# Kernel tuning notes

Measured on AMD Instinct MI355X. Metric: run time of the kernel, lower is better.

## Reference

```python
import jax, jax.numpy as jnp
import numpy as np

N_ORB = 1024    # Monte-Carlo orbits
NTIMES = 1024   # observation epochs
N_FZ = 24       # zodi flux grid points (uniform in log10)
N_KEZ = 6       # exozodi multipliers (sorted, searchsorted lookup)
N_TINT = 64     # integration times
N_ALPHA = 512   # separations (uniform in log10)


def setup_inputs() -> dict:
    key = jax.random.key(0)
    k1, k2, k3, k4 = jax.random.split(key, 4)
    fZs = jnp.logspace(-10.0, -7.0, N_FZ).astype(jnp.float32)
    alphas = jnp.logspace(-2.0, 1.0, N_ALPHA).astype(jnp.float32)
    kEZs = jnp.array([0.5, 1.0, 2.0, 5.0, 10.0, 20.0], dtype=jnp.float32)
    # grid already in the module's internal (n_fZ, n_kEZ, n_tint, n_alpha) layout
    grid = 25.0 + jax.random.normal(k1, (N_FZ, N_KEZ, N_TINT, N_ALPHA), dtype=jnp.float32)
    # alpha slightly exceeds [alphas[0], alphas[-1]] so geom_mask is exercised
    alpha = (10.0 ** jax.random.uniform(k2, (N_ORB, NTIMES), minval=-2.2, maxval=1.1)).astype(jnp.float32)
    dMag = (25.0 + jax.random.normal(k3, (N_ORB, NTIMES))).astype(jnp.float32)
    fZ_vals = (10.0 ** jax.random.uniform(k4, (NTIMES,), minval=-10.0, maxval=-7.0)).astype(jnp.float32)
    kEZ_val = jnp.float32(1.5)
    return dict(alpha=alpha, dMag=dMag, fZ_vals=fZ_vals, kEZ_val=kEZ_val,
                grid=grid, fZs=fZs, kEZs=kEZs, alphas=alphas)


def reference(alpha, dMag, fZ_vals, kEZ_val, grid, fZs, kEZs, alphas):
    """Faithful vectorized translation of dMag0Grid._pdet_alpha_dMag.

    alpha, dMag: (n_orb, ntimes); fZ_vals: (ntimes,); kEZ_val: scalar;
    grid: (n_fZ, n_kEZ, n_tint, n_alpha). Returns pdet (ntimes, n_tint).
    """
    n_fZ = fZs.shape[0]
    n_alpha = alphas.shape[0]
    log_fZs = jnp.log10(fZs)
    inv_log_fZ_step = 1.0 / (log_fZs[1] - log_fZs[0])
    log_alphas = jnp.log10(alphas)
    inv_log_alpha_step = 1.0 / (log_alphas[1] - log_alphas[0])

    geom_mask = (alpha >= alphas[0]) & (alpha <= alphas[-1])          # (n_orb, ntimes)

    fZ_ind = (jnp.log10(fZ_vals) - log_fZs[0]) * inv_log_fZ_step
    fZ0 = jnp.clip(jnp.floor(fZ_ind).astype(jnp.int32) + 1, 0, n_fZ - 2)  # (ntimes,)

    a_ind = (jnp.log10(alpha) - log_alphas[0]) * inv_log_alpha_step
    a0 = jnp.clip(a_ind.astype(jnp.int32), 0, n_alpha - 1)               # (n_orb, ntimes)
    dalpha = (a_ind - a0).astype(grid.dtype)

    kEZ_ind = jnp.searchsorted(kEZs, kEZ_val, side='right') - 1

    # lax.dynamic_slice clamps the start so the width-2 window fits:
    s = jnp.minimum(a0, n_alpha - 2)                                     # (n_orb, ntimes)

    g = jnp.take(grid, kEZ_ind, axis=1)                                  # (n_fZ, n_tint, n_alpha)
    g_f = g[fZ0]                                                          # (ntimes, n_tint, n_alpha)
    sT = s.T                                                              # (ntimes, n_orb)
    g0 = jnp.take_along_axis(g_f, sT[:, None, :], axis=2)                 # (ntimes, n_tint, n_orb)
    g1 = jnp.take_along_axis(g_f, (sT + 1)[:, None, :], axis=2)
    res = g0 + dalpha.T[:, None, :] * (g1 - g0)                           # (ntimes, n_tint, n_orb)

    dim = jnp.transpose(res, (2, 0, 1))                                   # (n_orb, ntimes, n_tint)
    det_mask = geom_mask[..., None] & jnp.signbit(dMag[..., None] - dim)
    pdet = det_mask.astype(jnp.float32).mean(axis=0)                      # (ntimes, n_tint)
    return pdet
```

## Files before the change

kernel.cpp:

```cpp
#include <hip/hip_runtime.h>
#include <math.h>

#define N_ORB   1024
#define NTIMES  1024
#define N_FZ    24
#define N_KEZ   6
#define N_TINT  64
#define N_ALPHA 512

#define GT_BYTES (N_FZ * N_ALPHA * N_TINT * 4)

__global__ __launch_bounds__(256) void stage_inputs(
    const float* __restrict__ grid, const float* __restrict__ kEZs,
    const float* __restrict__ kEZ_val_p, const float* __restrict__ alpha,
    const float* __restrict__ dMag, const float* __restrict__ alphas,
    float* __restrict__ gT, float4* __restrict__ P)
{
    __shared__ float lds[64 * 65];

    int b = blockIdx.x;
    if (b < 192) {
        float kv = kEZ_val_p[0];
        int cnt = 0;
#pragma unroll
        for (int i = 0; i < N_KEZ; ++i) cnt += (kEZs[i] <= kv) ? 1 : 0;
        int kez = cnt - 1;
        kez = kez < 0 ? 0 : (kez > N_KEZ - 1 ? N_KEZ - 1 : kez);

        int fz = b >> 3, sc = b & 7;
        int w = threadIdx.x >> 6, lane = threadIdx.x & 63;
        const float* gsrc = grid + ((size_t)fz * N_KEZ + kez) * N_TINT * N_ALPHA;

#pragma unroll
        for (int r = 0; r < 16; ++r) {
            int tint = w * 16 + r;
            lds[tint * 65 + lane] = gsrc[(size_t)tint * N_ALPHA + sc * 64 + lane];
        }
        __syncthreads();
#pragma unroll
        for (int r = 0; r < 16; ++r) {
            int sl = w * 16 + r;
            gT[((size_t)fz * N_ALPHA + sc * 64 + sl) * N_TINT + lane] = lds[lane * 65 + sl];
        }
    } else {
        float* da = lds;
        float* dm = lds + 1056;
        int*   of = (int*)(lds + 2112);

        int u = b - 192;
        int t0 = (u & 31) * 32, o0 = (u >> 5) * 32;
        int row = threadIdx.x >> 5, col = threadIdx.x & 31;

        float al0 = alphas[0], al1 = alphas[N_ALPHA - 1];
        float la0 = log10f(al0);
        float inv_step = 1.0f / (log10f(alphas[1]) - la0);

#pragma unroll
        for (int r = 0; r < 4; ++r) {
            int ol = r * 8 + row;
            size_t idx = (size_t)(o0 + ol) * NTIMES + t0 + col;
            float a = alpha[idx];
            float d = dMag[idx];
            float a_ind = (log10f(a) - la0) * inv_step;
            int a0i = (int)a_ind;
            a0i = a0i < 0 ? 0 : (a0i > N_ALPHA - 1 ? N_ALPHA - 1 : a0i);
            float dal = a_ind - (float)a0i;
            int s = a0i > N_ALPHA - 2 ? N_ALPHA - 2 : a0i;
            bool geom = (a >= al0) && (a <= al1);
            da[ol * 33 + col] = dal;
            dm[ol * 33 + col] = geom ? d : __builtin_inff();
            of[ol * 33 + col] = s * N_TINT;
        }
        __syncthreads();
#pragma unroll
        for (int r = 0; r < 4; ++r) {
            int tl = r * 8 + row;
            float4 v;
            v.x = da[col * 33 + tl];
            v.y = dm[col * 33 + tl];
            v.z = __int_as_float(of[col * 33 + tl]);
            v.w = 0.0f;
            P[(size_t)(t0 + tl) * N_ORB + o0 + col] = v;
        }
    }
}

__global__ __launch_bounds__(256) void pdet_main(
    const float* __restrict__ fZ_vals, const float* __restrict__ fZs,
    const float* __restrict__ gT, const float4* __restrict__ P,
    float* __restrict__ out)
{
    __shared__ float4 Psort[N_ORB];
    __shared__ int    hist[512];
    __shared__ int    histPS[512];
    __shared__ int    red[4 * 64];

    int t = blockIdx.x;
    int tid = threadIdx.x;
    int w = tid >> 6, lane = tid & 63;

    float lf0 = log10f(fZs[0]);
    float inv_f = 1.0f / (log10f(fZs[1]) - lf0);
    float fi = (log10f(fZ_vals[t]) - lf0) * inv_f;
    int f0 = (int)floorf(fi) + 1;
    f0 = f0 < 0 ? 0 : (f0 > N_FZ - 2 ? N_FZ - 2 : f0);

    const float*  gB = gT + (size_t)f0 * N_ALPHA * N_TINT;
    const float4* Pt = P + (size_t)t * N_ORB;

    hist[tid] = 0; hist[tid + 256] = 0;
    __syncthreads();

    float4 v[4];
    int    bin[4];
#pragma unroll
    for (int k = 0; k < 4; ++k) {
        v[k] = Pt[tid + k * 256];
        int s = __float_as_int(v[k].z) >> 6;
        bin[k] = isinf(v[k].y) ? 511 : s;
        atomicAdd(&hist[bin[k]], 1);
    }
    __syncthreads();

    if (tid < 64) {
        int pre[8]; int run = 0;
#pragma unroll
        for (int j = 0; j < 8; ++j) { pre[j] = run; run += hist[tid * 8 + j]; }
        int inc = run;
#pragma unroll
        for (int d = 1; d < 64; d <<= 1) {
            int n = __shfl_up(inc, d);
            if (lane >= d) inc += n;
        }
        int excl = inc - run;
#pragma unroll
        for (int j = 0; j < 8; ++j) histPS[tid * 8 + j] = excl + pre[j];
    }
    __syncthreads();

#pragma unroll
    for (int k = 0; k < 4; ++k) {
        int pos = atomicAdd(&histPS[bin[k]], 1);
        Psort[pos] = v[k];
    }
    __syncthreads();

    int q  = lane >> 4;
    int tg = (lane & 15) << 2;
    int base = w * 256;

    int c0 = 0, c1 = 0, c2 = 0, c3 = 0;

#pragma unroll 4
    for (int it = 0; it < 64; ++it) {
        float4 pd = Psort[base + it * 4 + q];
        float dal = pd.x, dm = pd.y;
        int offw = __float_as_int(pd.z);
        const float4* rowp = reinterpret_cast<const float4*>(gB + offw + tg);
        float4 g0 = rowp[0];
        float4 g1 = rowp[16];
        c0 += dm < fmaf(dal, g1.x - g0.x, g0.x);
        c1 += dm < fmaf(dal, g1.y - g0.y, g0.y);
        c2 += dm < fmaf(dal, g1.z - g0.z, g0.z);
        c3 += dm < fmaf(dal, g1.w - g0.w, g0.w);
    }

    c0 += __shfl_xor(c0, 16); c0 += __shfl_xor(c0, 32);
    c1 += __shfl_xor(c1, 16); c1 += __shfl_xor(c1, 32);
    c2 += __shfl_xor(c2, 16); c2 += __shfl_xor(c2, 32);
    c3 += __shfl_xor(c3, 16); c3 += __shfl_xor(c3, 32);

    if (lane < 16) {
        red[w * 64 + lane * 4 + 0] = c0;
        red[w * 64 + lane * 4 + 1] = c1;
        red[w * 64 + lane * 4 + 2] = c2;
        red[w * 64 + lane * 4 + 3] = c3;
    }
    __syncthreads();
    if (tid < 64) {
        int tot = red[tid] + red[64 + tid] + red[128 + tid] + red[192 + tid];
        out[(size_t)t * N_TINT + tid] = (float)tot * (1.0f / 1024.0f);
    }
}

extern "C" void kernel_launch(void* const* d_in, const int* in_sizes, int n_in,
                              void* d_out, int out_size, void* d_ws, size_t ws_size,
                              hipStream_t stream) {
    const float* alpha   = (const float*)d_in[0];
    const float* dMag    = (const float*)d_in[1];
    const float* fZ_vals = (const float*)d_in[2];
    const float* kEZ_val = (const float*)d_in[3];
    const float* grid    = (const float*)d_in[4];
    const float* fZs     = (const float*)d_in[5];
    const float* kEZs    = (const float*)d_in[6];
    const float* alphas  = (const float*)d_in[7];
    float*  out = (float*)d_out;

    float*  gT = (float*)d_ws;
    float4* P  = (float4*)((char*)d_ws + GT_BYTES);

    stage_inputs<<<dim3(192 + 1024), 256, 0, stream>>>(
        grid, kEZs, kEZ_val, alpha, dMag, alphas, gT, P);
    pdet_main<<<dim3(NTIMES), 256, 0, stream>>>(fZ_vals, fZs, gT, P, out);
}
```

Before: 104.6 us.

## Stage grid slice in LDS and process four fZ-sorted epochs per block

The prepass now sorts epochs by their fZ slice index into a list. Each 1024-thread block handles four epochs from that list, copying the whole 128KB grid slice into LDS with global_load_lds and reloading it only when the slice changes. Per-orbit data shrinks from float4 to float2 by packing index and fraction into one float, and the next epoch's tile is double-buffered. Gathers are served from LDS instead of global/L2 and the per-block histogram sort is dropped, at the cost of very high LDS use per block (occupancy of one block per CU) and packed 8-bit counters.

Measured after the change: 108.4 us. 3.6% more time.

```diff
diff --git a/kernel.cpp b/kernel.cpp
--- a/kernel.cpp
+++ b/kernel.cpp
@@ -8,17 +8,29 @@
 #define N_TINT  64
 #define N_ALPHA 512
 
-#define GT_BYTES (N_FZ * N_ALPHA * N_TINT * 4)
+#define SLICE_FLOATS (N_ALPHA * N_TINT)
+#define GT_BYTES (N_FZ * SLICE_FLOATS * 4)
+#define P_BYTES  (NTIMES * N_ORB * 8)
+
+typedef __attribute__((address_space(1))) const unsigned int gas_u32;
+typedef __attribute__((address_space(3))) unsigned int las_u32;
+
+__device__ __forceinline__ void gl_lds16(const float* g, float* l) {
+    __builtin_amdgcn_global_load_lds((gas_u32*)g, (las_u32*)l, 16, 0, 0);
+}
 
 __global__ __launch_bounds__(256) void stage_inputs(
     const float* __restrict__ grid, const float* __restrict__ kEZs,
     const float* __restrict__ kEZ_val_p, const float* __restrict__ alpha,
     const float* __restrict__ dMag, const float* __restrict__ alphas,
-    float* __restrict__ gT, float4* __restrict__ P)
+    const float* __restrict__ fZ_vals, const float* __restrict__ fZs,
+    float* __restrict__ gT, float2* __restrict__ P, int* __restrict__ t_list)
 {
     __shared__ float lds[64 * 65];
 
     int b = blockIdx.x;
+    int tid = threadIdx.x;
+
     if (b < 192) {
         float kv = kEZ_val_p[0];
         int cnt = 0;
@@ -28,7 +40,7 @@
         kez = kez < 0 ? 0 : (kez > N_KEZ - 1 ? N_KEZ - 1 : kez);
 
         int fz = b >> 3, sc = b & 7;
-        int w = threadIdx.x >> 6, lane = threadIdx.x & 63;
+        int w = tid >> 6, lane = tid & 63;
         const float* gsrc = grid + ((size_t)fz * N_KEZ + kez) * N_TINT * N_ALPHA;
 
 #pragma unroll
@@ -42,14 +54,13 @@
             int sl = w * 16 + r;
             gT[((size_t)fz * N_ALPHA + sc * 64 + sl) * N_TINT + lane] = lds[lane * 65 + sl];
         }
-    } else {
-        float* da = lds;
-        float* dm = lds + 1056;
-        int*   of = (int*)(lds + 2112);
+    } else if (b < 192 + 1024) {
+        float* xa  = lds;
+        float* dmv = lds + 1056;
 
         int u = b - 192;
-        int t0 = (u & 31) * 32, o0 = (u >> 5) * 32;
-        int row = threadIdx.x >> 5, col = threadIdx.x & 31;
+        int t0 = (u & 31) << 5, o0 = (u >> 5) << 5;
+        int row = tid >> 5, col = tid & 31;
 
         float al0 = alphas[0], al1 = alphas[N_ALPHA - 1];
         float la0 = log10f(al0);
@@ -57,129 +68,168 @@
 
 #pragma unroll
         for (int r = 0; r < 4; ++r) {
-            int ol = r * 8 + row;
+            int ol = (r << 3) + row;
             size_t idx = (size_t)(o0 + ol) * NTIMES + t0 + col;
             float a = alpha[idx];
             float d = dMag[idx];
             float a_ind = (log10f(a) - la0) * inv_step;
-            int a0i = (int)a_ind;
-            a0i = a0i < 0 ? 0 : (a0i > N_ALPHA - 1 ? N_ALPHA - 1 : a0i);
-            float dal = a_ind - (float)a0i;
-            int s = a0i > N_ALPHA - 2 ? N_ALPHA - 2 : a0i;
             bool geom = (a >= al0) && (a <= al1);
-            da[ol * 33 + col] = dal;
-            dm[ol * 33 + col] = geom ? d : __builtin_inff();
-            of[ol * 33 + col] = s * N_TINT;
+            float x = a_ind;
+            if (a_ind >= 511.0f) x = a_ind - 1.0f;
+            if (!geom) x = 0.0f;
+            x = fmaxf(x, 0.0f);
+            xa[ol * 33 + col]  = x;
+            dmv[ol * 33 + col] = geom ? d : __builtin_inff();
         }
         __syncthreads();
 #pragma unroll
         for (int r = 0; r < 4; ++r) {
-            int tl = r * 8 + row;
-            float4 v;
-            v.x = da[col * 33 + tl];
-            v.y = dm[col * 33 + tl];
-            v.z = __int_as_float(of[col * 33 + tl]);
-            v.w = 0.0f;
+            int tl = (r << 3) + row;
+            float2 v;
+            v.x = xa[col * 33 + tl];
+            v.y = dmv[col * 33 + tl];
             P[(size_t)(t0 + tl) * N_ORB + o0 + col] = v;
         }
-    }
-}
-
-__global__ __launch_bounds__(256) void pdet_main(
+    } else {
+        __shared__ int h[32];
+        __shared__ int ps[32];
+        if (tid < 32) h[tid] = 0;
+        __syncthreads();
+
+        float lf0 = log10f(fZs[0]);
+        float inv_f = 1.0f / (log10f(fZs[1]) - lf0);
+        int f0r[4];
+#pragma unroll
+        for (int k = 0; k < 4; ++k) {
+            int t = tid + (k << 8);
+            float fi = (log10f(fZ_vals[t]) - lf0) * inv_f;
+            int f0 = (int)floorf(fi) + 1;
+            f0 = f0 < 0 ? 0 : (f0 > N_FZ - 2 ? N_FZ - 2 : f0);
+            f0r[k] = f0;
+            atomicAdd(&h[f0], 1);
+        }
+        __syncthreads();
+        if (tid == 0) {
+            int run = 0;
+#pragma unroll
+            for (int i = 0; i < N_FZ; ++i) { ps[i] = run; run += h[i]; }
+        }
+        __syncthreads();
+#pragma unroll
+        for (int k = 0; k < 4; ++k) {
+            int pos = atomicAdd(&ps[f0r[k]], 1);
+            t_list[pos] = tid + (k << 8);
+        }
+    }
+}
+
+__global__ __launch_bounds__(1024) void pdet_main(
     const float* __restrict__ fZ_vals, const float* __restrict__ fZs,
-    const float* __restrict__ gT, const float4* __restrict__ P,
-    float* __restrict__ out)
+    const float* __restrict__ gT, const float2* __restrict__ P,
+    const int* __restrict__ t_list, float* __restrict__ out)
 {
-    __shared__ float4 Psort[N_ORB];
-    __shared__ int    hist[512];
-    __shared__ int    histPS[512];
-    __shared__ int    red[4 * 64];
-
-    int t = blockIdx.x;
-    int tid = threadIdx.x;
-    int w = tid >> 6, lane = tid & 63;
-
-    float lf0 = log10f(fZs[0]);
-    float inv_f = 1.0f / (log10f(fZs[1]) - lf0);
-    float fi = (log10f(fZ_vals[t]) - lf0) * inv_f;
-    int f0 = (int)floorf(fi) + 1;
-    f0 = f0 < 0 ? 0 : (f0 > N_FZ - 2 ? N_FZ - 2 : f0);
-
-    const float*  gB = gT + (size_t)f0 * N_ALPHA * N_TINT;
-    const float4* Pt = P + (size_t)t * N_ORB;
-
-    hist[tid] = 0; hist[tid + 256] = 0;
+    __shared__ float  g_lds[SLICE_FLOATS];
+    __shared__ float2 Ptile[2][N_ORB];
+    __shared__ uint2  red[16][64];
+    __shared__ int    tsh[4];
+
+    const int tid  = threadIdx.x;
+    const int w    = tid >> 6;
+    const int lane = tid & 63;
+    const int hh   = lane >> 5;
+    const int tp   = lane & 31;
+    const int tb   = blockIdx.x << 2;
+
+    const float lf0   = log10f(fZs[0]);
+    const float inv_f = 1.0f / (log10f(fZs[1]) - lf0);
+
+    if (tid < 4) tsh[tid] = t_list[tb + tid];
+
+    int t0 = t_list[tb];
+    float fi = (log10f(fZ_vals[t0]) - lf0) * inv_f;
+    int staged = (int)floorf(fi) + 1;
+    staged = staged < 0 ? 0 : (staged > N_FZ - 2 ? N_FZ - 2 : staged);
+    {
+        const float* src = gT + (size_t)staged * SLICE_FLOATS;
+#pragma unroll
+        for (int r = 0; r < 8; ++r) {
+            int chunk = (r << 4) + w;
+            gl_lds16(src + (chunk << 8) + (lane << 2), &g_lds[chunk << 8]);
+        }
+    }
+    if (w < 8) {
+        const float* src = (const float*)(P + (size_t)t0 * N_ORB);
+        gl_lds16(src + (w << 8) + (lane << 2), (float*)&Ptile[0][0] + (w << 8));
+    }
     __syncthreads();
 
-    float4 v[4];
-    int    bin[4];
-#pragma unroll
-    for (int k = 0; k < 4; ++k) {
-        v[k] = Pt[tid + k * 256];
-        int s = __float_as_int(v[k].z) >> 6;
-        bin[k] = isinf(v[k].y) ? 511 : s;
-        atomicAdd(&hist[bin[k]], 1);
-    }
+    unsigned Aacc = 0, Bacc = 0;
+    const int obase = w << 6;
+
+#pragma unroll
+    for (int q = 0; q < 4; ++q) {
+        if (q < 3 && w < 8) {
+            int tn = t_list[tb + q + 1];
+            const float* src = (const float*)(P + (size_t)tn * N_ORB);
+            gl_lds16(src + (w << 8) + (lane << 2),
+                     (float*)&Ptile[(q + 1) & 1][0] + (w << 8));
+        }
+
+        const float2* Pb = Ptile[q & 1];
+        int ca = 0, cb = 0;
+#pragma unroll 8
+        for (int j = 0; j < 32; ++j) {
+            float2 pd = Pb[obase + (j << 1) + hh];
+            int   si  = (int)pd.x;
+            float dal = pd.x - (float)si;
+            int   idx = (si << 6) + (tp << 1);
+            float2 r0 = *(const float2*)&g_lds[idx];
+            float2 r1 = *(const float2*)&g_lds[idx + 64];
+            ca += pd.y < fmaf(dal, r1.x - r0.x, r0.x);
+            cb += pd.y < fmaf(dal, r1.y - r0.y, r0.y);
+        }
+        Aacc |= (unsigned)ca << (q << 3);
+        Bacc |= (unsigned)cb << (q << 3);
+
+        __syncthreads();
+
+        if (q < 3) {
+            int tn = t_list[tb + q + 1];
+            float fin = (log10f(fZ_vals[tn]) - lf0) * inv_f;
+            int f0n = (int)floorf(fin) + 1;
+            f0n = f0n < 0 ? 0 : (f0n > N_FZ - 2 ? N_FZ - 2 : f0n);
+            if (f0n != staged) {
+                const float* src = gT + (size_t)f0n * SLICE_FLOATS;
+#pragma unroll
+                for (int r = 0; r < 8; ++r) {
+                    int chunk = (r << 4) + w;
+                    gl_lds16(src + (chunk << 8) + (lane << 2), &g_lds[chunk << 8]);
+                }
+                staged = f0n;
+                __syncthreads();
+            }
+        }
+    }
+
+    red[w][lane] = make_uint2(Aacc, Bacc);
     __syncthreads();
 
-    if (tid < 64) {
-        int pre[8]; int run = 0;
-#pragma unroll
-        for (int j = 0; j < 8; ++j) { pre[j] = run; run += hist[tid * 8 + j]; }
-        int inc = run;
-#pragma unroll
-        for (int d = 1; d < 64; d <<= 1) {
-            int n = __shfl_up(inc, d);
-            if (lane >= d) inc += n;
-        }
-        int excl = inc - run;
-#pragma unroll
-        for (int j = 0; j < 8; ++j) histPS[tid * 8 + j] = excl + pre[j];
-    }
-    __syncthreads();
-
-#pragma unroll
-    for (int k = 0; k < 4; ++k) {
-        int pos = atomicAdd(&histPS[bin[k]], 1);
-        Psort[pos] = v[k];
-    }
-    __syncthreads();
-
-    int q  = lane >> 4;
-    int tg = (lane & 15) << 2;
-    int base = w * 256;
-
-    int c0 = 0, c1 = 0, c2 = 0, c3 = 0;
-
-#pragma unroll 4
-    for (int it = 0; it < 64; ++it) {
-        float4 pd = Psort[base + it * 4 + q];
-        float dal = pd.x, dm = pd.y;
-        int offw = __float_as_int(pd.z);
-        const float4* rowp = reinterpret_cast<const float4*>(gB + offw + tg);
-        float4 g0 = rowp[0];
-        float4 g1 = rowp[16];
-        c0 += dm < fmaf(dal, g1.x - g0.x, g0.x);
-        c1 += dm < fmaf(dal, g1.y - g0.y, g0.y);
-        c2 += dm < fmaf(dal, g1.z - g0.z, g0.z);
-        c3 += dm < fmaf(dal, g1.w - g0.w, g0.w);
-    }
-
-    c0 += __shfl_xor(c0, 16); c0 += __shfl_xor(c0, 32);
-    c1 += __shfl_xor(c1, 16); c1 += __shfl_xor(c1, 32);
-    c2 += __shfl_xor(c2, 16); c2 += __shfl_xor(c2, 32);
-    c3 += __shfl_xor(c3, 16); c3 += __shfl_xor(c3, 32);
-
-    if (lane < 16) {
-        red[w * 64 + lane * 4 + 0] = c0;
-        red[w * 64 + lane * 4 + 1] = c1;
-        red[w * 64 + lane * 4 + 2] = c2;
-        red[w * 64 + lane * 4 + 3] = c3;
-    }
-    __syncthreads();
-    if (tid < 64) {
-        int tot = red[tid] + red[64 + tid] + red[128 + tid] + red[192 + tid];
-        out[(size_t)t * N_TINT + tid] = (float)tot * (1.0f / 1024.0f);
+    if (tid < 256) {
+        const int tq  = tid >> 6;
+        const int ti  = tid & 63;
+        const int tpp = ti >> 1;
+        const int e   = ti & 1;
+        int sum = 0;
+#pragma unroll
+        for (int ww = 0; ww < 16; ++ww) {
+            uint2 v0 = red[ww][tpp];
+            uint2 v1 = red[ww][32 + tpp];
+            unsigned u0 = e ? v0.y : v0.x;
+            unsigned u1 = e ? v1.y : v1.x;
+            sum += (int)((u0 >> (tq << 3)) & 255u);
+            sum += (int)((u1 >> (tq << 3)) & 255u);
+        }
+        out[(size_t)tsh[tq] * N_TINT + ti] = (float)sum * (1.0f / 1024.0f);
     }
 }
 
@@ -194,12 +244,13 @@
     const float* fZs     = (const float*)d_in[5];
     const float* kEZs    = (const float*)d_in[6];
     const float* alphas  = (const float*)d_in[7];
-    float*  out = (float*)d_out;
-
-    float*  gT = (float*)d_ws;
-    float4* P  = (float4*)((char*)d_ws + GT_BYTES);
-
-    stage_inputs<<<dim3(192 + 1024), 256, 0, stream>>>(
-        grid, kEZs, kEZ_val, alpha, dMag, alphas, gT, P);
-    pdet_main<<<dim3(NTIMES), 256, 0, stream>>>(fZ_vals, fZs, gT, P, out);
-}
+    float* out = (float*)d_out;
+
+    float*  gT     = (float*)d_ws;
+    float2* P      = (float2*)((char*)d_ws + GT_BYTES);
+    int*    t_list = (int*)((char*)d_ws + GT_BYTES + P_BYTES);
+
+    stage_inputs<<<dim3(192 + 1024 + 1), 256, 0, stream>>>(
+        grid, kEZs, kEZ_val, alpha, dMag, alphas, fZ_vals, fZs, gT, P, t_list);
+    pdet_main<<<dim3(256), 1024, 0, stream>>>(fZ_vals, fZs, gT, P, t_list, out);
+}
```
